# Optimization experiments

Hardware: AMD Instinct MI355X
Metric: run time of the kernel (lower is better)

## Reference

```python
import jax, jax.numpy as jnp
import numpy as np

B, N, E, M = 512, 101, 128, 8
DK = E // M  # 16
EPS = 1e-5

def _bn(x, g, b):
    # torch BatchNorm1d in train mode on (B, E, N): per-channel stats over batch+city dims, biased var
    mu = jnp.mean(x, axis=(0, 1))
    var = jnp.mean((x - mu) ** 2, axis=(0, 1))
    return (x - mu) * jax.lax.rsqrt(var + EPS) * g + b

def setup_inputs() -> dict:
    key = jax.random.key(0)
    ks = jax.random.split(key, 24)
    sc = 1.0 / np.sqrt(E)
    inp = {
        's': jax.random.uniform(ks[0], (B, N, 2), jnp.float32),
        'd': jax.random.randint(ks[1], (B, N, 1), 0, 10),
        'e_w': jax.random.normal(ks[2], (3, E), jnp.float32) * sc,
        'e_b': jax.random.normal(ks[3], (E,), jnp.float32) * sc,
        'ep_w': jax.random.normal(ks[4], (2, E), jnp.float32) * sc,
        'ep_b': jax.random.normal(ks[5], (E,), jnp.float32) * sc,
        'Wq': jax.random.normal(ks[6], (3, E, E), jnp.float32) * sc,
        'bq': jax.random.normal(ks[7], (3, E), jnp.float32) * sc,
        'Wk': jax.random.normal(ks[8], (3, E, E), jnp.float32) * sc,
        'bk': jax.random.normal(ks[9], (3, E), jnp.float32) * sc,
        'Wv': jax.random.normal(ks[10], (3, E, E), jnp.float32) * sc,
        'bv': jax.random.normal(ks[11], (3, E), jnp.float32) * sc,
        'Wo': jax.random.normal(ks[12], (3, E, E), jnp.float32) * sc,
        'bo': jax.random.normal(ks[13], (3, E), jnp.float32) * sc,
        'Wf1': jax.random.normal(ks[14], (3, E, 4 * E), jnp.float32) * sc,
        'bf1': jax.random.normal(ks[15], (3, 4 * E), jnp.float32) * sc,
        'Wf2': jax.random.normal(ks[16], (3, 4 * E, E), jnp.float32) * sc,
        'bf2': jax.random.normal(ks[17], (3, E), jnp.float32) * sc,
        'g1': jnp.ones((3, E), jnp.float32),
        'be1': jnp.zeros((3, E), jnp.float32),
        'g2': jnp.ones((3, E), jnp.float32),
        'be2': jnp.zeros((3, E), jnp.float32),
    }
    return inp

def reference(s, d, e_w, e_b, ep_w, ep_b, Wq, bq, Wk, bk, Wv, bv, Wo, bo,
              Wf1, bf1, Wf2, bf2, g1, be1, g2, be2):
    # node embedding: cat(coords, demand) -> Linear(3,E); depot row uses Linear(2,E)
    sss = jnp.concatenate([s, d.astype(s.dtype)], axis=2)          # (B,N,3)
    node = sss @ e_w + e_b                                         # (B,N,E)
    node = node.at[:, 0, :].set(s[:, 0, :] @ ep_w + ep_b)
    x = node
    inv_sqrt_dk = 1.0 / (DK ** 0.5)
    for i in range(3):
        res = x
        q = (x @ Wq[i] + bq[i]).reshape(B, N, M, DK)
        k = (x @ Wk[i] + bk[i]).reshape(B, N, M, DK)
        v = (x @ Wv[i] + bv[i]).reshape(B, N, M, DK)
        # scores[b,i,j,h] = <q_i, k_j> per head (source does expand*mul*sum)
        scores = jnp.einsum('bihd,bjhd->bijh', q, k) * inv_sqrt_dk  # (B,N,N,M)
        a = jax.nn.softmax(scores, axis=2)                          # over keys j
        o = jnp.einsum('bijh,bjhd->bihd', a, v).reshape(B, N, E)
        x = _bn(o @ Wo[i] + bo[i] + res, g1[i], be1[i])
        ff = jax.nn.relu(x @ Wf1[i] + bf1[i]) @ Wf2[i] + bf2[i]
        x = _bn(x + ff, g2[i], be2[i])
    return x
```

## Files before the change

kernel.cpp:

```cpp
#include <hip/hip_runtime.h>
#include <hip/hip_fp16.h>
#include <stdint.h>

#define TROWS 51712
#define NCITY 101
#define BATCH 512
#define EDIM  128
#define NBH   4096

using half_t = _Float16;
typedef __attribute__((ext_vector_type(8))) _Float16 h8;
typedef __attribute__((ext_vector_type(4))) _Float16 h4;
typedef __attribute__((ext_vector_type(4))) float   f32x4;

typedef __attribute__((address_space(1))) const unsigned int gu32;
typedef __attribute__((address_space(3))) unsigned int lu32;
static __device__ __forceinline__ void async16(const void* g, const void* l) {
    __builtin_amdgcn_global_load_lds((gu32*)g, (lu32*)(uint32_t)(uintptr_t)l, 16, 0, 0);
}

static __device__ __forceinline__ int swz_col(int c, int row) {
    return (c & ~31) | ((((c >> 3) ^ (row >> 1)) & 3) << 3) | (c & 7);
}

__global__ __launch_bounds__(256)
void prep_kernel(const float* __restrict__ Wq, const float* __restrict__ Wk,
                 const float* __restrict__ Wv, const float* __restrict__ Wo,
                 const float* __restrict__ Wf1, const float* __restrict__ Wf2,
                 const float* __restrict__ bq, const float* __restrict__ bk,
                 const float* __restrict__ bv,
                 half_t* __restrict__ wqkv, half_t* __restrict__ wo,
                 half_t* __restrict__ wf1, half_t* __restrict__ wf2,
                 float* __restrict__ bqkv)
{
    const int which = blockIdx.y;
    const int gid = blockIdx.x * 256 + threadIdx.x;
    if (which <= 2) {
        if (gid >= 3 * 128 * 128) return;
        const float* src = (which == 0) ? Wq : (which == 1) ? Wk : Wv;
        int l = gid >> 14, r = gid & 16383, k = r >> 7, n = r & 127;
        wqkv[(size_t)l * 49152 + which * 16384 + n * 128 + swz_col(k, n)] = (half_t)src[gid];
    } else if (which == 3) {
        if (gid >= 3 * 128 * 128) return;
        int l = gid >> 14, r = gid & 16383, k = r >> 7, n = r & 127;
        wo[(size_t)l * 16384 + n * 128 + swz_col(k, n)] = (half_t)Wo[gid];
    } else if (which == 4) {
        if (gid >= 3 * 65536) return;
        int l = gid >> 16, u = gid & 65535;
        int j = u >> 13, kc = (u >> 11) & 3, n = (u >> 5) & 63, hp = u & 31;
        int k = kc * 32 + ((((hp >> 3) ^ (n >> 1)) & 3) << 3) + (hp & 7);
        wf1[(size_t)l * 65536 + u] = (half_t)Wf1[(size_t)(l * 128 + k) * 512 + j * 64 + n];
    } else if (which == 5) {
        if (gid >= 3 * 65536) return;
        int l = gid >> 16, u = gid & 65535;
        int j = u >> 13, kc = (u >> 12) & 1, n = (u >> 5) & 127, hp = u & 31;
        int kh = j * 64 + kc * 32 + ((((hp >> 3) ^ (n >> 1)) & 3) << 3) + (hp & 7);
        wf2[(size_t)l * 65536 + u] = (half_t)Wf2[(size_t)(l * 512 + kh) * 128 + n];
    } else {
        if (gid >= 3 * 384) return;
        int l = gid / 384, c = gid - l * 384;
        float v = (c < 128) ? bq[l * 128 + c]
                : (c < 256) ? bk[l * 128 + c - 128]
                            : bv[l * 128 + c - 256];
        bqkv[gid] = v;
    }
}

__global__ __launch_bounds__(256)
void embed_kernel(const float* __restrict__ s, const int* __restrict__ d,
                  const float* __restrict__ e_w, const float* __restrict__ e_b,
                  const float* __restrict__ ep_w, const float* __restrict__ ep_b,
                  half_t* __restrict__ xh)
{
    int gid = blockIdx.x * 256 + threadIdx.x;
    int row = gid >> 7;
    int c   = gid & 127;
    int b = row / NCITY;
    int n = row - b * NCITY;
    const float* sp = s + ((size_t)b * NCITY + n) * 2;
    float v;
    if (n == 0) {
        v = sp[0] * ep_w[c] + sp[1] * ep_w[128 + c] + ep_b[c];
    } else {
        float dv = (float)d[b * NCITY + n];
        v = sp[0] * e_w[c] + sp[1] * e_w[128 + c] + dv * e_w[256 + c] + e_b[c];
    }
    xh[(size_t)row * 128 + swz_col(c, row)] = (half_t)v;
}

__global__ __launch_bounds__(256)
void qkv_gemm(const half_t* __restrict__ A, const half_t* __restrict__ B,
              const float* __restrict__ bias,
              half_t* __restrict__ outQ, half_t* __restrict__ outK,
              half_t* __restrict__ outV)
{
    constexpr int K = 128;
    __shared__ alignas(16) half_t smem[128 * 136];
    half_t* sA = smem;
    half_t* sB = smem + 8192;

    const int tid  = threadIdx.x;
    const int wave = tid >> 6, lane = tid & 63;
    const int n0 = blockIdx.x * 128;
    const int m0 = blockIdx.y * 128;

    const int sr = wave * 16 + (lane >> 2);
    const int sc = (lane & 3) * 8;
    const half_t* gA = A + (size_t)(m0 + sr) * K + sc;
    const half_t* gB = B + (size_t)(n0 + sr) * K + sc;
    const int ldst = wave * 512;

    const int quad = lane >> 4, l16 = lane & 15;
    const int wm = (wave >> 1) * 64, wn = (wave & 1) * 64;

    f32x4 acc[4][4] = {};

    async16(gA,                  &sA[ldst]);
    async16(gA + (size_t)64 * K, &sA[2048 + ldst]);
    async16(gB,                  &sB[ldst]);
    async16(gB + (size_t)64 * K, &sB[2048 + ldst]);

    for (int ks = 0; ks < 4; ++ks) {
        __syncthreads();
        if (ks + 1 < 4) {
            const int k0 = (ks + 1) * 32;
            const int nb = (ks + 1) & 1;
            async16(gA + k0,                  &sA[nb * 4096 + ldst]);
            async16(gA + (size_t)64 * K + k0, &sA[nb * 4096 + 2048 + ldst]);
            async16(gB + k0,                  &sB[nb * 4096 + ldst]);
            async16(gB + (size_t)64 * K + k0, &sB[nb * 4096 + 2048 + ldst]);
        }
        const int cb = ks & 1;
        h8 af[4], bf[4];
        #pragma unroll
        for (int mi = 0; mi < 4; ++mi) {
            int r = wm + mi * 16 + l16;
            af[mi] = *(const h8*)(&sA[cb * 4096 + r * 32 + (((quad ^ (r >> 1)) & 3) << 3)]);
        }
        #pragma unroll
        for (int ni = 0; ni < 4; ++ni) {
            int n = wn + ni * 16 + l16;
            bf[ni] = *(const h8*)(&sB[cb * 4096 + n * 32 + (((quad ^ (n >> 1)) & 3) << 3)]);
        }
        #pragma unroll
        for (int mi = 0; mi < 4; ++mi)
        #pragma unroll
        for (int ni = 0; ni < 4; ++ni)
            acc[mi][ni] = __builtin_amdgcn_mfma_f32_16x16x32_f16(af[mi], bf[ni], acc[mi][ni], 0, 0, 0);
    }

    __syncthreads();
    half_t* sT = smem;
    #pragma unroll
    for (int ni = 0; ni < 4; ++ni) {
        int col = wn + ni * 16 + l16;
        float bvv = bias[n0 + col];
        #pragma unroll
        for (int mi = 0; mi < 4; ++mi) {
            #pragma unroll
            for (int r = 0; r < 4; ++r) {
                int row = wm + mi * 16 + quad * 4 + r;
                int g = (col >> 3) ^ ((row & 8) >> 2);
                sT[row * 136 + g * 8 + (col & 7)] = (half_t)(acc[mi][ni][r] + bvv);
            }
        }
    }
    __syncthreads();
    half_t* dst = (blockIdx.x == 0) ? outQ : (blockIdx.x == 1) ? outK : outV;
    #pragma unroll
    for (int i = 0; i < 8; ++i) {
        int u = tid + 256 * i;
        int row = u >> 4, chunk = u & 15;
        int g = chunk ^ ((row & 8) >> 2);
        h8 v = *(const h8*)(&sT[row * 136 + g * 8]);
        int rg = m0 + row;
        int bb = rg / NCITY, tok = rg - bb * NCITY;
        *(h8*)(dst + ((size_t)(bb * 8 + (chunk >> 1)) * NCITY + tok) * 16 + (chunk & 1) * 8) = v;
    }
}

__global__ __launch_bounds__(512, 2)
void attn_oproj(const half_t* __restrict__ Qh, const half_t* __restrict__ Kh,
                const half_t* __restrict__ V,  const half_t* __restrict__ wo,
                const float* __restrict__ bo,  const half_t* __restrict__ xh,
                half_t* __restrict__ y16, float* __restrict__ stats)
{
    __shared__ alignas(16) half_t sO[112 * 136];

    const int b    = blockIdx.x;
    const int wave = threadIdx.x >> 6;
    const int bh   = b * 8 + wave;
    const int lane = threadIdx.x & 63, quad = lane >> 4, l16 = lane & 15;
    const int s0 = (((quad & 1) * 2)    ) * 16 + l16;
    const int s1 = (((quad & 1) * 2) + 1) * 16 + l16;
    const bool hi2 = (quad >> 1) != 0;

    const half_t* qbase = Qh + (size_t)bh * NCITY * 16;
    const half_t* kbase = Kh + (size_t)bh * NCITY * 16;
    const half_t* vbase = V  + (size_t)bh * NCITY * 16;

    h8 kf[7];
    #pragma unroll
    for (int jt = 0; jt < 7; ++jt) {
        kf[jt] = (h8){};
        if (quad < 2)
            kf[jt] = *reinterpret_cast<const h8*>(kbase + (jt * 16 + l16) * 16 + quad * 8);
    }
    h8 vt[4];
    #pragma unroll
    for (int p = 0; p < 4; ++p)
        #pragma unroll
        for (int jj = 0; jj < 8; ++jj)
            vt[p][jj] = vbase[(size_t)(p * 32 + quad * 8 + jj) * 16 + l16];

    h8 qf = {};
    if (quad < 2)
        qf = *reinterpret_cast<const h8*>(qbase + l16 * 16 + quad * 8);

    const int ocol = wave * 16 + l16;

    for (int it = 0; it < 7; ++it) {
        h8 qn = {};
        if (it < 6 && quad < 2)
            qn = *reinterpret_cast<const h8*>(qbase + ((it + 1) * 16 + l16) * 16 + quad * 8);

        f32x4 S[7];
        #pragma unroll
        for (int jt = 0; jt < 7; ++jt) {
            f32x4 a = {};
            a = __builtin_amdgcn_mfma_f32_16x16x32_f16(kf[jt], qf, a, 0, 0, 0);
            S[jt] = a;
        }
        float m = -1e30f;
        #pragma unroll
        for (int jt = 0; jt < 7; ++jt)
            #pragma unroll
            for (int r = 0; r < 4; ++r) {
                int jg = jt * 16 + quad * 4 + r;
                float sv = (jg < NCITY) ? S[jt][r] * 0.25f : -1e30f;
                S[jt][r] = sv;
                m = fmaxf(m, sv);
            }
        m = fmaxf(m, __shfl_xor(m, 16));
        m = fmaxf(m, __shfl_xor(m, 32));
        float sum = 0.0f;
        #pragma unroll
        for (int jt = 0; jt < 7; ++jt)
            #pragma unroll
            for (int r = 0; r < 4; ++r) {
                float e = __expf(S[jt][r] - m);
                S[jt][r] = e;
                sum += e;
            }
        sum += __shfl_xor(sum, 16);
        sum += __shfl_xor(sum, 32);
        float inv = 1.0f / sum;
        #pragma unroll
        for (int jt = 0; jt < 7; ++jt)
            #pragma unroll
            for (int r = 0; r < 4; ++r) S[jt][r] *= inv;

        f32x4 O = {};
        #pragma unroll
        for (int p = 0; p < 4; ++p) {
            float pj[8];
            #pragma unroll
            for (int r = 0; r < 4; ++r) {
                float a0 = __shfl(S[2 * p][r],     s0);
                float b0 = __shfl(S[2 * p + 1][r], s0);
                float a1 = __shfl(S[2 * p][r],     s1);
                float b1 = __shfl(S[2 * p + 1][r], s1);
                pj[r]     = hi2 ? b0 : a0;
                pj[4 + r] = hi2 ? b1 : a1;
            }
            h8 ph;
            #pragma unroll
            for (int jj = 0; jj < 8; ++jj)
                ph[jj] = (half_t)pj[jj];
            O = __builtin_amdgcn_mfma_f32_16x16x32_f16(ph, vt[p], O, 0, 0, 0);
        }
        #pragma unroll
        for (int r = 0; r < 4; ++r) {
            int q = it * 16 + quad * 4 + r;
            int g = (ocol >> 3) ^ ((q & 8) >> 2);
            sO[q * 136 + g * 8 + (ocol & 7)] = (half_t)O[r];
        }
        qf = qn;
    }
    __syncthreads();

    h8 bfr[4];
    {
        const half_t* wrow = wo + (size_t)ocol * 128;
        const int nsw = (ocol >> 1) & 3;
        #pragma unroll
        for (int kc = 0; kc < 4; ++kc)
            bfr[kc] = *(const h8*)(wrow + kc * 32 + (((quad ^ nsw) & 3) << 3));
    }
    f32x4 acc[7];
    #pragma unroll
    for (int mi = 0; mi < 7; ++mi) {
        acc[mi] = (f32x4){};
        int row = mi * 16 + l16;
        int swr = (row & 8) >> 2;
        #pragma unroll
        for (int kc = 0; kc < 4; ++kc) {
            h8 af = *(const h8*)(&sO[row * 136 + (((kc * 4 + quad) ^ swr) << 3)]);
            acc[mi] = __builtin_amdgcn_mfma_f32_16x16x32_f16(af, bfr[kc], acc[mi], 0, 0, 0);
        }
    }
    float bvv = bo[ocol];
    float s = 0.0f, ss = 0.0f;
    #pragma unroll
    for (int mi = 0; mi < 7; ++mi) {
        #pragma unroll
        for (int r = 0; r < 4; ++r) {
            int q = mi * 16 + quad * 4 + r;
            if (q < NCITY) {
                size_t grow = (size_t)b * NCITY + q;
                float o = acc[mi][r] + bvv + (float)xh[grow * 128 + swz_col(ocol, (int)grow)];
                y16[grow * 128 + ocol] = (half_t)o;
                s += o; ss += o * o;
            }
        }
    }
    s  += __shfl_xor(s, 16);  s  += __shfl_xor(s, 32);
    ss += __shfl_xor(ss, 16); ss += __shfl_xor(ss, 32);
    if (quad == 0) {
        atomicAdd(&stats[ocol], s);
        atomicAdd(&stats[128 + ocol], ss);
    }
}

__global__ __launch_bounds__(512, 4)
void ff_fused(half_t* __restrict__ y16, const float* __restrict__ st1,
              const float* __restrict__ g1, const float* __restrict__ be1,
              const half_t* __restrict__ w1, const half_t* __restrict__ w2,
              const float* __restrict__ bf1, const float* __restrict__ bf2,
              float* __restrict__ stats)
{
    __shared__ alignas(16) half_t sX[4][128 * 32];
    __shared__ alignas(16) half_t sW1f[8192];
    __shared__ alignas(16) half_t sW2f[8192];
    __shared__ alignas(16) half_t sH[2][128 * 32];

    const int tid  = threadIdx.x;
    const int wave = tid >> 6, lane = tid & 63;
    const int quad = lane >> 4, l16 = lane & 15;
    const int m0 = blockIdx.x * 128;
    const int wr = wave >> 1;
    const int wc = wave & 1;

    const float invN = 1.0f / (float)TROWS;
    const int so = wave * 512 + lane * 8;

    h8 rw1a = *(const h8*)(w1 + so);
    h8 rw1b = *(const h8*)(w1 + so + 4096);
    h8 rw2a = *(const h8*)(w2 + so);
    h8 rw2b = *(const h8*)(w2 + so + 4096);

    float* sBN = (float*)&sW1f[0];
    if (tid < 128) {
        float mean = st1[tid] * invN;
        float var  = st1[128 + tid] * invN - mean * mean;
        float scl  = g1[tid] * rsqrtf(var + 1e-5f);
        sBN[tid]       = scl;
        sBN[128 + tid] = be1[tid] - mean * scl;
    }
    __syncthreads();

    {
        const int row = tid >> 2;
        const int q   = tid & 3;
        const int qs  = ((q ^ (row >> 1)) & 3) << 3;
        const half_t* src = y16 + (size_t)(m0 + row) * 128 + q * 8;
        #pragma unroll
        for (int kc = 0; kc < 4; ++kc) {
            h8 v = *(const h8*)(src + kc * 32);
            h8 xv;
            #pragma unroll
            for (int r = 0; r < 8; ++r) {
                int c = kc * 32 + q * 8 + r;
                xv[r] = (half_t)((float)v[r] * sBN[c] + sBN[128 + c]);
            }
            *(h8*)(&sX[kc][row * 32 + qs]) = xv;
        }
    }

    f32x4 acc2[2][4] = {};

    for (int j = 0; j < 8; ++j) {
        asm volatile("s_waitcnt lgkmcnt(0)" ::: "memory");
        __builtin_amdgcn_s_barrier();
        __builtin_amdgcn_sched_barrier(0);
        *(h8*)(&sW1f[so])        = rw1a;
        *(h8*)(&sW1f[so + 4096]) = rw1b;
        *(h8*)(&sW2f[so])        = rw2a;
        *(h8*)(&sW2f[so + 4096]) = rw2b;
        asm volatile("s_waitcnt lgkmcnt(0)" ::: "memory");
        __builtin_amdgcn_s_barrier();
        __builtin_amdgcn_sched_barrier(0);
        if (j < 7) {
            const half_t* w1n = w1 + (size_t)(j + 1) * 8192;
            const half_t* w2n = w2 + (size_t)(j + 1) * 8192;
            rw1a = *(const h8*)(w1n + so);
            rw1b = *(const h8*)(w1n + so + 4096);
            rw2a = *(const h8*)(w2n + so);
            rw2b = *(const h8*)(w2n + so + 4096);
        }

        f32x4 acc1[2][2] = {};
        #pragma unroll
        for (int kc = 0; kc < 4; ++kc) {
            h8 af[2], bf[2];
            #pragma unroll
            for (int mi = 0; mi < 2; ++mi) {
                int r = wr * 32 + mi * 16 + l16;
                af[mi] = *(const h8*)(&sX[kc][r * 32 + (((quad ^ (r >> 1)) & 3) << 3)]);
            }
            #pragma unroll
            for (int ni = 0; ni < 2; ++ni) {
                int n = wc * 32 + ni * 16 + l16;
                bf[ni] = *(const h8*)(&sW1f[kc * 2048 + n * 32 + (((quad ^ (n >> 1)) & 3) << 3)]);
            }
            #pragma unroll
            for (int mi = 0; mi < 2; ++mi)
            #pragma unroll
            for (int ni = 0; ni < 2; ++ni)
                acc1[mi][ni] = __builtin_amdgcn_mfma_f32_16x16x32_f16(af[mi], bf[ni], acc1[mi][ni], 0, 0, 0);
        }
        #pragma unroll
        for (int ni = 0; ni < 2; ++ni) {
            int c = wc * 32 + ni * 16 + l16;
            float bvv = bf1[j * 64 + c];
            int kc2 = c >> 5, c5 = c & 31;
            #pragma unroll
            for (int mi = 0; mi < 2; ++mi)
            #pragma unroll
            for (int r = 0; r < 4; ++r) {
                int row = wr * 32 + mi * 16 + quad * 4 + r;
                float v = acc1[mi][ni][r] + bvv;
                v = v > 0.0f ? v : 0.0f;
                int hsw = (c5 & 7) | ((((c5 >> 3) ^ (row >> 1)) & 3) << 3);
                sH[kc2][row * 32 + hsw] = (half_t)v;
            }
        }
        asm volatile("s_waitcnt lgkmcnt(0)" ::: "memory");
        __builtin_amdgcn_s_barrier();
        __builtin_amdgcn_sched_barrier(0);

        #pragma unroll
        for (int kc = 0; kc < 2; ++kc) {
            h8 af[2], bf[4];
            #pragma unroll
            for (int mi = 0; mi < 2; ++mi) {
                int r = wr * 32 + mi * 16 + l16;
                af[mi] = *(const h8*)(&sH[kc][r * 32 + (((quad ^ (r >> 1)) & 3) << 3)]);
            }
            #pragma unroll
            for (int ni = 0; ni < 4; ++ni) {
                int n = wc * 64 + ni * 16 + l16;
                bf[ni] = *(const h8*)(&sW2f[kc * 4096 + n * 32 + (((quad ^ (n >> 1)) & 3) << 3)]);
            }
            #pragma unroll
            for (int mi = 0; mi < 2; ++mi)
            #pragma unroll
            for (int ni = 0; ni < 4; ++ni)
                acc2[mi][ni] = __builtin_amdgcn_mfma_f32_16x16x32_f16(af[mi], bf[ni], acc2[mi][ni], 0, 0, 0);
        }
    }

    __syncthreads();
    float* red = (float*)&sH[0][0];

    #pragma unroll
    for (int ni = 0; ni < 4; ++ni) {
        int col = wc * 64 + ni * 16 + l16;
        float bvv = bf2[col];
        int kc = col >> 5, c5 = col & 31;
        float s = 0.0f, ss = 0.0f;
        #pragma unroll
        for (int mi = 0; mi < 2; ++mi) {
            #pragma unroll
            for (int r = 0; r < 4; ++r) {
                int rowl = wr * 32 + mi * 16 + quad * 4 + r;
                int hsw = (c5 & 7) | ((((c5 >> 3) ^ (rowl >> 1)) & 3) << 3);
                float xv = (float)sX[kc][rowl * 32 + hsw];
                float o = acc2[mi][ni][r] + bvv + xv;
                y16[(size_t)(m0 + rowl) * 128 + col] = (half_t)o;
                s += o; ss += o * o;
            }
        }
        s  += __shfl_xor(s, 16);  s  += __shfl_xor(s, 32);
        ss += __shfl_xor(ss, 16); ss += __shfl_xor(ss, 32);
        if (quad == 0) {
            red[wave * 64 + ni * 16 + l16]       = s;
            red[512 + wave * 64 + ni * 16 + l16] = ss;
        }
    }
    __syncthreads();
    if (tid < 256) {
        int a   = tid >> 7;
        int col = tid & 127;
        int wcc = col >> 6, nii = (col >> 4) & 3, lx = col & 15;
        float t = 0.0f;
        #pragma unroll
        for (int w = 0; w < 4; ++w)
            t += red[a * 512 + (w * 2 + wcc) * 64 + nii * 16 + lx];
        atomicAdd(&stats[a * 128 + col], t);
    }
}

__global__ __launch_bounds__(256)
void bn_apply(const h8* __restrict__ y, const float* __restrict__ stats,
              const float* __restrict__ g, const float* __restrict__ be,
              half_t* __restrict__ xh, float* __restrict__ dst32)
{
    __shared__ float sh[256];
    const int tid = threadIdx.x;
    if (tid < 128) {
        const float invN = 1.0f / (float)TROWS;
        float mean = stats[tid] * invN;
        float var  = stats[128 + tid] * invN - mean * mean;
        float inv  = rsqrtf(var + 1e-5f);
        float scl  = g[tid] * inv;
        sh[tid]       = scl;
        sh[128 + tid] = be[tid] - mean * scl;
    }
    __syncthreads();

    int gid = blockIdx.x * 256 + tid;
    int row = gid >> 4;
    int gr  = gid & 15;
    int c = gr * 8;
    h8 v = y[gid];
    h8 hv;
    float o[8];
    #pragma unroll
    for (int r = 0; r < 8; ++r) {
        o[r] = (float)v[r] * sh[c + r] + sh[128 + c + r];
        hv[r] = (half_t)o[r];
    }
    int grp = (gr & ~3) | ((gr ^ (row >> 1)) & 3);
    *reinterpret_cast<h8*>(xh + (size_t)row * 128 + grp * 8) = hv;
    if (dst32) {
        f32x4 lo = { o[0], o[1], o[2], o[3] };
        f32x4 hi = { o[4], o[5], o[6], o[7] };
        ((f32x4*)dst32)[gid * 2]     = lo;
        ((f32x4*)dst32)[gid * 2 + 1] = hi;
    }
}

extern "C" void kernel_launch(void* const* d_in, const int* in_sizes, int n_in,
                              void* d_out, int out_size, void* d_ws, size_t ws_size,
                              hipStream_t stream)
{
    const float* s    = (const float*)d_in[0];
    const int*   dd   = (const int*)d_in[1];
    const float* e_w  = (const float*)d_in[2];
    const float* e_b  = (const float*)d_in[3];
    const float* ep_w = (const float*)d_in[4];
    const float* ep_b = (const float*)d_in[5];
    const float* Wq   = (const float*)d_in[6];
    const float* bq   = (const float*)d_in[7];
    const float* Wk   = (const float*)d_in[8];
    const float* bk   = (const float*)d_in[9];
    const float* Wv   = (const float*)d_in[10];
    const float* bv   = (const float*)d_in[11];
    const float* Wo   = (const float*)d_in[12];
    const float* bo   = (const float*)d_in[13];
    const float* Wf1  = (const float*)d_in[14];
    const float* bf1  = (const float*)d_in[15];
    const float* Wf2  = (const float*)d_in[16];
    const float* bf2  = (const float*)d_in[17];
    const float* g1   = (const float*)d_in[18];
    const float* be1  = (const float*)d_in[19];
    const float* g2   = (const float*)d_in[20];
    const float* be2  = (const float*)d_in[21];

    char* ws = (char*)d_ws;
    size_t off = 0;
    auto alloc = [&](size_t bytes) -> void* {
        void* p = ws + off;
        off += (bytes + 255) & ~(size_t)255;
        return p;
    };
    half_t* y16   = (half_t*)alloc((size_t)TROWS * 128 * 2);
    half_t* xh    = (half_t*)alloc((size_t)TROWS * 128 * 2);
    half_t* Qh    = (half_t*)alloc((size_t)NBH * NCITY * 16 * 2);
    half_t* Kh    = (half_t*)alloc((size_t)NBH * NCITY * 16 * 2);
    half_t* Vb    = (half_t*)alloc((size_t)NBH * NCITY * 16 * 2);
    half_t* wqkv  = (half_t*)alloc((size_t)3 * 384 * 128 * 2);
    half_t* wo    = (half_t*)alloc((size_t)3 * 128 * 128 * 2);
    half_t* wf1   = (half_t*)alloc((size_t)3 * 512 * 128 * 2);
    half_t* wf2   = (half_t*)alloc((size_t)3 * 128 * 512 * 2);
    float*  bqkv  = (float*) alloc((size_t)3 * 384 * 4);
    float*  stats = (float*) alloc(6 * 256 * 4);

    dim3 blk(256);

    hipMemsetAsync(stats, 0, 6 * 256 * 4, stream);

    prep_kernel<<<dim3(768, 7), blk, 0, stream>>>(Wq, Wk, Wv, Wo, Wf1, Wf2, bq, bk, bv,
                                                  wqkv, wo, wf1, wf2, bqkv);

    embed_kernel<<<dim3(TROWS * 128 / 256), blk, 0, stream>>>(s, dd, e_w, e_b, ep_w, ep_b, xh);

    for (int l = 0; l < 3; ++l) {
        float* st1 = stats + (size_t)(l * 2) * 256;
        float* st2 = stats + (size_t)(l * 2 + 1) * 256;
        qkv_gemm<<<dim3(3, 404), blk, 0, stream>>>(xh, wqkv + (size_t)l * 49152,
                                                   bqkv + l * 384, Qh, Kh, Vb);
        attn_oproj<<<dim3(BATCH), dim3(512), 0, stream>>>(Qh, Kh, Vb,
                                                          wo + (size_t)l * 16384,
                                                          bo + l * 128, xh, y16, st1);
        ff_fused<<<dim3(404), dim3(512), 0, stream>>>(y16, st1, g1 + l * 128, be1 + l * 128,
                                                      wf1 + (size_t)l * 65536, wf2 + (size_t)l * 65536,
                                                      bf1 + l * 512, bf2 + l * 128, st2);
        bn_apply<<<dim3(TROWS * 16 / 256), blk, 0, stream>>>((const h8*)y16, st2,
                                                             g2 + l * 128, be2 + l * 128,
                                                             xh, (l == 2) ? (float*)d_out : nullptr);
    }
}
```

Before: 395.7 us.

## Fuse QKV projection into per-batch attention kernel via shared memory

Replaces the separate QKV GEMM kernel with an in-kernel projection: each batch block loads its 101 token rows of x into LDS, computes Q, K and V per head with MFMA, and writes them to swizzled LDS buffers that the attention and output-projection stages then read. This removes the global-memory write and read of the full Q/K/V tensors and one kernel launch per layer. In exchange, LDS use per block rises to roughly 116KB and launch bounds drop to one block per CU, which lowers occupancy and latency hiding. The QKV weights are also re-read by every batch block.

```diff
diff --git a/kernel.cpp b/kernel.cpp
--- a/kernel.cpp
+++ b/kernel.cpp
@@ -88,141 +88,108 @@
     xh[(size_t)row * 128 + swz_col(c, row)] = (half_t)v;
 }
 
-__global__ __launch_bounds__(256)
-void qkv_gemm(const half_t* __restrict__ A, const half_t* __restrict__ B,
-              const float* __restrict__ bias,
-              half_t* __restrict__ outQ, half_t* __restrict__ outK,
-              half_t* __restrict__ outV)
-{
-    constexpr int K = 128;
-    __shared__ alignas(16) half_t smem[128 * 136];
-    half_t* sA = smem;
-    half_t* sB = smem + 8192;
-
-    const int tid  = threadIdx.x;
-    const int wave = tid >> 6, lane = tid & 63;
-    const int n0 = blockIdx.x * 128;
-    const int m0 = blockIdx.y * 128;
-
-    const int sr = wave * 16 + (lane >> 2);
-    const int sc = (lane & 3) * 8;
-    const half_t* gA = A + (size_t)(m0 + sr) * K + sc;
-    const half_t* gB = B + (size_t)(n0 + sr) * K + sc;
-    const int ldst = wave * 512;
-
-    const int quad = lane >> 4, l16 = lane & 15;
-    const int wm = (wave >> 1) * 64, wn = (wave & 1) * 64;
-
-    f32x4 acc[4][4] = {};
-
-    async16(gA,                  &sA[ldst]);
-    async16(gA + (size_t)64 * K, &sA[2048 + ldst]);
-    async16(gB,                  &sB[ldst]);
-    async16(gB + (size_t)64 * K, &sB[2048 + ldst]);
-
-    for (int ks = 0; ks < 4; ++ks) {
-        __syncthreads();
-        if (ks + 1 < 4) {
-            const int k0 = (ks + 1) * 32;
-            const int nb = (ks + 1) & 1;
-            async16(gA + k0,                  &sA[nb * 4096 + ldst]);
-            async16(gA + (size_t)64 * K + k0, &sA[nb * 4096 + 2048 + ldst]);
-            async16(gB + k0,                  &sB[nb * 4096 + ldst]);
-            async16(gB + (size_t)64 * K + k0, &sB[nb * 4096 + 2048 + ldst]);
-        }
-        const int cb = ks & 1;
-        h8 af[4], bf[4];
-        #pragma unroll
-        for (int mi = 0; mi < 4; ++mi) {
-            int r = wm + mi * 16 + l16;
-            af[mi] = *(const h8*)(&sA[cb * 4096 + r * 32 + (((quad ^ (r >> 1)) & 3) << 3)]);
-        }
-        #pragma unroll
-        for (int ni = 0; ni < 4; ++ni) {
-            int n = wn + ni * 16 + l16;
-            bf[ni] = *(const h8*)(&sB[cb * 4096 + n * 32 + (((quad ^ (n >> 1)) & 3) << 3)]);
-        }
-        #pragma unroll
-        for (int mi = 0; mi < 4; ++mi)
-        #pragma unroll
-        for (int ni = 0; ni < 4; ++ni)
-            acc[mi][ni] = __builtin_amdgcn_mfma_f32_16x16x32_f16(af[mi], bf[ni], acc[mi][ni], 0, 0, 0);
-    }
-
-    __syncthreads();
-    half_t* sT = smem;
-    #pragma unroll
-    for (int ni = 0; ni < 4; ++ni) {
-        int col = wn + ni * 16 + l16;
-        float bvv = bias[n0 + col];
-        #pragma unroll
-        for (int mi = 0; mi < 4; ++mi) {
-            #pragma unroll
-            for (int r = 0; r < 4; ++r) {
-                int row = wm + mi * 16 + quad * 4 + r;
-                int g = (col >> 3) ^ ((row & 8) >> 2);
-                sT[row * 136 + g * 8 + (col & 7)] = (half_t)(acc[mi][ni][r] + bvv);
-            }
-        }
-    }
-    __syncthreads();
-    half_t* dst = (blockIdx.x == 0) ? outQ : (blockIdx.x == 1) ? outK : outV;
-    #pragma unroll
-    for (int i = 0; i < 8; ++i) {
-        int u = tid + 256 * i;
-        int row = u >> 4, chunk = u & 15;
-        int g = chunk ^ ((row & 8) >> 2);
-        h8 v = *(const h8*)(&sT[row * 136 + g * 8]);
-        int rg = m0 + row;
-        int bb = rg / NCITY, tok = rg - bb * NCITY;
-        *(h8*)(dst + ((size_t)(bb * 8 + (chunk >> 1)) * NCITY + tok) * 16 + (chunk & 1) * 8) = v;
-    }
-}
-
-__global__ __launch_bounds__(512, 2)
-void attn_oproj(const half_t* __restrict__ Qh, const half_t* __restrict__ Kh,
-                const half_t* __restrict__ V,  const half_t* __restrict__ wo,
-                const float* __restrict__ bo,  const half_t* __restrict__ xh,
-                half_t* __restrict__ y16, float* __restrict__ stats)
+__global__ __launch_bounds__(512, 1)
+void layer_attn(const half_t* __restrict__ xh, const half_t* __restrict__ wqkv,
+                const float* __restrict__ bqkv, const half_t* __restrict__ wo,
+                const float* __restrict__ bo, half_t* __restrict__ y16,
+                float* __restrict__ stats)
 {
     __shared__ alignas(16) half_t sO[112 * 136];
-
-    const int b    = blockIdx.x;
-    const int wave = threadIdx.x >> 6;
-    const int bh   = b * 8 + wave;
-    const int lane = threadIdx.x & 63, quad = lane >> 4, l16 = lane & 15;
+    __shared__ alignas(16) half_t sQKV[3][8][112 * 16];
+    half_t* sX = sO;
+
+    const int b   = blockIdx.x;
+    const int tid = threadIdx.x;
+    const int wave = tid >> 6, lane = tid & 63;
+    const int quad = lane >> 4, l16 = lane & 15;
+
+    if (tid < 448) {
+        int row = tid >> 2, kc = tid & 3;
+        h8* dst = (h8*)&sX[kc * 3584 + row * 32];
+        if (row < NCITY) {
+            size_t grow = (size_t)b * NCITY + row;
+            const h8* src = (const h8*)(xh + grow * 128 + kc * 32);
+            int xf = (int)(((grow >> 1) ^ (row >> 1)) & 3);
+            h8 v0 = src[0], v1 = src[1], v2 = src[2], v3 = src[3];
+            dst[0 ^ xf] = v0;
+            dst[1 ^ xf] = v1;
+            dst[2 ^ xf] = v2;
+            dst[3 ^ xf] = v3;
+        } else {
+            h8 z = {};
+            dst[0] = z; dst[1] = z; dst[2] = z; dst[3] = z;
+        }
+    }
+    __syncthreads();
+
+    const int hn  = wave * 16 + l16;
+    const int nsw = (hn >> 1) & 3;
+    h8 bfr[3][4];
+    float bv3[3];
+    #pragma unroll
+    for (int which = 0; which < 3; ++which) {
+        const half_t* wrow = wqkv + which * 16384 + (size_t)hn * 128;
+        #pragma unroll
+        for (int kc = 0; kc < 4; ++kc)
+            bfr[which][kc] = *(const h8*)(wrow + kc * 32 + (((quad ^ nsw) & 3) << 3));
+        bv3[which] = bqkv[which * 128 + hn];
+    }
+    #pragma unroll
+    for (int mi = 0; mi < 7; ++mi) {
+        h8 af[4];
+        #pragma unroll
+        for (int kc = 0; kc < 4; ++kc) {
+            int r = mi * 16 + l16;
+            af[kc] = *(const h8*)(&sX[kc * 3584 + r * 32 + (((quad ^ (r >> 1)) & 3) << 3)]);
+        }
+        #pragma unroll
+        for (int which = 0; which < 3; ++which) {
+            f32x4 a = {};
+            #pragma unroll
+            for (int kc = 0; kc < 4; ++kc)
+                a = __builtin_amdgcn_mfma_f32_16x16x32_f16(af[kc], bfr[which][kc], a, 0, 0, 0);
+            half_t* dstL = &sQKV[which][wave][0];
+            #pragma unroll
+            for (int r = 0; r < 4; ++r) {
+                int tok = mi * 16 + quad * 4 + r;
+                int dsw = l16 ^ (((tok >> 2) & 1) << 3);
+                dstL[tok * 16 + dsw] = (half_t)(a[r] + bv3[which]);
+            }
+        }
+    }
+    __syncthreads();
+
+    const half_t* qb = &sQKV[0][wave][0];
+    const half_t* kb = &sQKV[1][wave][0];
+    const half_t* vb = &sQKV[2][wave][0];
+    const int kflip = (l16 >> 2) & 1;
+
     const int s0 = (((quad & 1) * 2)    ) * 16 + l16;
     const int s1 = (((quad & 1) * 2) + 1) * 16 + l16;
     const bool hi2 = (quad >> 1) != 0;
 
-    const half_t* qbase = Qh + (size_t)bh * NCITY * 16;
-    const half_t* kbase = Kh + (size_t)bh * NCITY * 16;
-    const half_t* vbase = V  + (size_t)bh * NCITY * 16;
-
     h8 kf[7];
     #pragma unroll
     for (int jt = 0; jt < 7; ++jt) {
         kf[jt] = (h8){};
         if (quad < 2)
-            kf[jt] = *reinterpret_cast<const h8*>(kbase + (jt * 16 + l16) * 16 + quad * 8);
+            kf[jt] = *(const h8*)(kb + (jt * 16 + l16) * 16 + ((quad ^ kflip) << 3));
     }
     h8 vt[4];
     #pragma unroll
     for (int p = 0; p < 4; ++p)
         #pragma unroll
-        for (int jj = 0; jj < 8; ++jj)
-            vt[p][jj] = vbase[(size_t)(p * 32 + quad * 8 + jj) * 16 + l16];
-
-    h8 qf = {};
-    if (quad < 2)
-        qf = *reinterpret_cast<const h8*>(qbase + l16 * 16 + quad * 8);
-
-    const int ocol = wave * 16 + l16;
+        for (int jj = 0; jj < 8; ++jj) {
+            int tok = p * 32 + quad * 8 + jj;
+            vt[p][jj] = vb[tok * 16 + (l16 ^ (((jj >> 2) & 1) << 3))];
+        }
+
+    const int ocol = hn;
 
     for (int it = 0; it < 7; ++it) {
-        h8 qn = {};
-        if (it < 6 && quad < 2)
-            qn = *reinterpret_cast<const h8*>(qbase + ((it + 1) * 16 + l16) * 16 + quad * 8);
+        h8 qf = {};
+        if (quad < 2)
+            qf = *(const h8*)(qb + (it * 16 + l16) * 16 + ((quad ^ kflip) << 3));
 
         f32x4 S[7];
         #pragma unroll
@@ -285,17 +252,16 @@
             int g = (ocol >> 3) ^ ((q & 8) >> 2);
             sO[q * 136 + g * 8 + (ocol & 7)] = (half_t)O[r];
         }
-        qf = qn;
-    }
-    __syncthreads();
-
-    h8 bfr[4];
+    }
+    __syncthreads();
+
+    h8 bfr2[4];
     {
         const half_t* wrow = wo + (size_t)ocol * 128;
-        const int nsw = (ocol >> 1) & 3;
+        const int nsw2 = (ocol >> 1) & 3;
         #pragma unroll
         for (int kc = 0; kc < 4; ++kc)
-            bfr[kc] = *(const h8*)(wrow + kc * 32 + (((quad ^ nsw) & 3) << 3));
+            bfr2[kc] = *(const h8*)(wrow + kc * 32 + (((quad ^ nsw2) & 3) << 3));
     }
     f32x4 acc[7];
     #pragma unroll
@@ -306,7 +272,7 @@
         #pragma unroll
         for (int kc = 0; kc < 4; ++kc) {
             h8 af = *(const h8*)(&sO[row * 136 + (((kc * 4 + quad) ^ swr) << 3)]);
-            acc[mi] = __builtin_amdgcn_mfma_f32_16x16x32_f16(af, bfr[kc], acc[mi], 0, 0, 0);
+            acc[mi] = __builtin_amdgcn_mfma_f32_16x16x32_f16(af, bfr2[kc], acc[mi], 0, 0, 0);
         }
     }
     float bvv = bo[ocol];
@@ -587,9 +553,6 @@
     };
     half_t* y16   = (half_t*)alloc((size_t)TROWS * 128 * 2);
     half_t* xh    = (half_t*)alloc((size_t)TROWS * 128 * 2);
-    half_t* Qh    = (half_t*)alloc((size_t)NBH * NCITY * 16 * 2);
-    half_t* Kh    = (half_t*)alloc((size_t)NBH * NCITY * 16 * 2);
-    half_t* Vb    = (half_t*)alloc((size_t)NBH * NCITY * 16 * 2);
     half_t* wqkv  = (half_t*)alloc((size_t)3 * 384 * 128 * 2);
     half_t* wo    = (half_t*)alloc((size_t)3 * 128 * 128 * 2);
     half_t* wf1   = (half_t*)alloc((size_t)3 * 512 * 128 * 2);
@@ -609,11 +572,10 @@
     for (int l = 0; l < 3; ++l) {
         float* st1 = stats + (size_t)(l * 2) * 256;
         float* st2 = stats + (size_t)(l * 2 + 1) * 256;
-        qkv_gemm<<<dim3(3, 404), blk, 0, stream>>>(xh, wqkv + (size_t)l * 49152,
-                                                   bqkv + l * 384, Qh, Kh, Vb);
-        attn_oproj<<<dim3(BATCH), dim3(512), 0, stream>>>(Qh, Kh, Vb,
+        layer_attn<<<dim3(BATCH), dim3(512), 0, stream>>>(xh, wqkv + (size_t)l * 49152,
+                                                          bqkv + l * 384,
                                                           wo + (size_t)l * 16384,
-                                                          bo + l * 128, xh, y16, st1);
+                                                          bo + l * 128, y16, st1);
         ff_fused<<<dim3(404), dim3(512), 0, stream>>>(y16, st1, g1 + l * 128, be1 + l * 128,
                                                       wf1 + (size_t)l * 65536, wf2 + (size_t)l * 65536,
                                                       bf1 + l * 512, bf2 + l * 128, st2);
```

Result: no change. 391.8 us (-1.0%).
